# Kernel tuning notes

Hardware: AMD Instinct MI355X
Metric: run time of the kernel (lower is better)

## Reference

```python
import jax, jax.numpy as jnp
import numpy as np

D_MODEL = 1024
N_HEADS = 16
D_K = D_MODEL // N_HEADS
SEQ = 2048
BATCH = 4


def setup_inputs() -> dict:
    key = jax.random.key(0)
    ks = jax.random.split(key, 11)
    s = 0.02
    inp = {
        'query': jax.random.normal(ks[0], (SEQ, BATCH, D_MODEL), jnp.float32),
        'key': jax.random.normal(ks[1], (SEQ, BATCH, D_MODEL), jnp.float32),
        'value': jax.random.normal(ks[2], (SEQ, BATCH, D_MODEL), jnp.float32),
        'Wq': jax.random.normal(ks[3], (D_MODEL, D_MODEL), jnp.float32) * s,
        'bq': jnp.zeros((D_MODEL,), jnp.float32),
        'Wk': jax.random.normal(ks[4], (D_MODEL, D_MODEL), jnp.float32) * s,
        'bk': jnp.zeros((D_MODEL,), jnp.float32),
        'Wv': jax.random.normal(ks[5], (D_MODEL, D_MODEL), jnp.float32) * s,
        'bv': jnp.zeros((D_MODEL,), jnp.float32),
        'Wo': jax.random.normal(ks[6], (D_MODEL, D_MODEL), jnp.float32) * s,
        'bo': jnp.zeros((D_MODEL,), jnp.float32),
    }
    return inp


def reference(query, key, value, Wq, bq, Wk, bk, Wv, bv, Wo, bo):
    # inputs are [S, B, D]; module transposes to batch-first
    q_in = jnp.swapaxes(query, 0, 1)  # [B, S, D]
    k_in = jnp.swapaxes(key, 0, 1)
    v_in = jnp.swapaxes(value, 0, 1)
    B, S, _ = q_in.shape
    # torch Linear: x @ W.T + b
    q = (q_in @ Wq.T + bq).reshape(B, S, N_HEADS, D_K)
    k = (k_in @ Wk.T + bk).reshape(B, S, N_HEADS, D_K)
    v = (v_in @ Wv.T + bv).reshape(B, S, N_HEADS, D_K)
    scale = jnp.sqrt(jnp.float32(D_K))
    scores = jnp.einsum('bqhd,bkhd->bhqk', q, k) / scale  # [B, H, S, S]
    attn = jax.nn.softmax(scores, axis=-1)
    # dropout is identity in eval / p=0
    context = jnp.einsum('bhqk,bkhd->bqhd', attn, v).reshape(B, S, D_MODEL)
    out = context @ Wo.T + bo  # [B, S, D]
    return jnp.swapaxes(out, 0, 1)  # back to [S, B, D]
```

## Files before the change

kernel.cpp:

```cpp
#include <hip/hip_runtime.h>
#include <math.h>

typedef unsigned short u16;
typedef unsigned int   u32;
typedef float f32x4  __attribute__((ext_vector_type(4)));
typedef float f32x16 __attribute__((ext_vector_type(16)));
typedef __bf16 bf16x8 __attribute__((ext_vector_type(8)));
typedef __bf16 bf16x2 __attribute__((ext_vector_type(2)));

#define SEQ   2048
#define BATCH 4
#define NH    16
#define DK    64
#define DM    1024
#define MTOT  (SEQ*BATCH)
#define SCL_QK 0.18033688011116016f

#if __has_builtin(__builtin_amdgcn_exp2f)
#define EXP2(x) __builtin_amdgcn_exp2f(x)
#else
#define EXP2(x) exp2f(x)
#endif

static __device__ __forceinline__ u16 f2bf(float f) {
  __bf16 h = (__bf16)f;
  return __builtin_bit_cast(u16, h);
}
static __device__ __forceinline__ u32 pk2(float a, float b) {
  bf16x2 t = {(__bf16)a, (__bf16)b};
  return __builtin_bit_cast(u32, t);
}

typedef __attribute__((address_space(1))) const void g1_t;
typedef __attribute__((address_space(3))) void l3_t;
static __device__ __forceinline__ void gload16(const void* g, void* l) {
  __builtin_amdgcn_global_load_lds((g1_t*)g, (l3_t*)l, 16, 0, 0);
}

static __device__ __forceinline__ void cast8(const float* __restrict__ src,
                                             u16* __restrict__ dst, int i) {
  float4 a = ((const float4*)src)[2 * i];
  float4 b = ((const float4*)src)[2 * i + 1];
  uint4 r;
  r.x = pk2(a.x, a.y); r.y = pk2(a.z, a.w);
  r.z = pk2(b.x, b.y); r.w = pk2(b.z, b.w);
  ((uint4*)dst)[i] = r;
}

__global__ __launch_bounds__(256)
void cast_bf16(const float* __restrict__ src, u16* __restrict__ dst, int n8) {
  int i = blockIdx.x * 256 + threadIdx.x;
  if (i < n8) cast8(src, dst, i);
}

__global__ __launch_bounds__(256)
void cast_w(const float* __restrict__ Wq, const float* __restrict__ Wk,
            const float* __restrict__ Wv, const float* __restrict__ Wo,
            u16* __restrict__ w3, u16* __restrict__ wo_c) {
  int bid = blockIdx.x;
  int t = bid >> 9, idx = bid & 511;
  const float* src = (t == 0) ? Wq : (t == 1) ? Wk : (t == 2) ? Wv : Wo;
  u16* dst = (t < 3) ? (w3 + (size_t)t * DM * DM) : wo_c;
  cast8(src, dst, idx * 256 + threadIdx.x);
}

__global__ __launch_bounds__(256)
void cast_all(const float* __restrict__ q, const float* __restrict__ k,
              const float* __restrict__ v,
              const float* __restrict__ Wq, const float* __restrict__ Wk,
              const float* __restrict__ Wv, const float* __restrict__ Wo,
              u16* __restrict__ in_c, u16* __restrict__ w3, u16* __restrict__ wo_c) {
  int bid = blockIdx.x;
  const float* src; u16* dst; int idx;
  if (bid < 12288) {
    int t = bid >> 12; idx = bid & 4095;
    src = (t == 0) ? q : (t == 1) ? k : v;
    dst = in_c + (size_t)t * MTOT * DM;
  } else {
    int wb = bid - 12288;
    int t = wb >> 9; idx = wb & 511;
    src = (t == 0) ? Wq : (t == 1) ? Wk : (t == 2) ? Wv : Wo;
    dst = (t < 3) ? (w3 + (size_t)t * DM * DM) : wo_c;
  }
  cast8(src, dst, idx * 256 + threadIdx.x);
}

template<int OGEMM>
__global__ __launch_bounds__(256, 4)
void gemm_k(const u16* __restrict__ a0, const u16* __restrict__ a1,
            const u16* __restrict__ a2, const u16* __restrict__ w3,
            const float* __restrict__ b0, const float* __restrict__ b1,
            const float* __restrict__ b2,
            u16* __restrict__ o0, u16* __restrict__ o1, u16* __restrict__ o2,
            float* __restrict__ o3, int seg_base)
{
  constexpr int BM = 128, BN = 128, BK = 32;
  __shared__ u16 As[BM * BK];
  __shared__ u16 Bs[BN * BK];

  const int seg = OGEMM ? 0 : (seg_base + (int)(blockIdx.x >> 3));
  const int n0  = OGEMM ? blockIdx.x * BN : (blockIdx.x & 7) * BN;
  const int m0  = blockIdx.y * BM;
  const u16* A = OGEMM ? a0 : (seg == 0 ? a0 : seg == 1 ? a1 : a2);
  const u16* W = OGEMM ? w3 : (w3 + (size_t)seg * DM * DM);
  const float* bias = OGEMM ? b0 : (seg == 0 ? b0 : seg == 1 ? b1 : b2);

  const int tid  = threadIdx.x;
  const int w    = tid >> 6;
  const int lane = tid & 63;
  const int quad = lane >> 4;
  const int l15  = lane & 15;
  const int wm = (w >> 1) * 64;
  const int wn = (w & 1) * 64;

  size_t aoff[2], woff[2];
  for (int p = 0; p < 2; p++) {
    int row = w * 32 + p * 16 + (lane >> 2);
    int gm = m0 + row;
    if (OGEMM) {
      aoff[p] = (size_t)gm * DM + (lane & 3) * 8;
    } else {
      int bb = gm >> 11, s = gm & (SEQ - 1);
      aoff[p] = (size_t)(s * BATCH + bb) * DM + (lane & 3) * 8;
    }
    woff[p] = (size_t)(n0 + row) * DM + (lane & 3) * 8;
  }

  f32x4 zero4 = {0.f, 0.f, 0.f, 0.f};
  f32x4 acc[4][4];
  for (int i = 0; i < 4; i++)
    for (int j = 0; j < 4; j++)
      acc[i][j] = zero4;

  for (int k0 = 0; k0 < DM; k0 += BK) {
    for (int p = 0; p < 2; p++) {
      gload16(A + aoff[p] + k0, &As[(w * 32 + p * 16) * BK]);
      gload16(W + woff[p] + k0, &Bs[(w * 32 + p * 16) * BK]);
    }
    __syncthreads();
    bf16x8 af[4], bfr[4];
    for (int i = 0; i < 4; i++)
      af[i] = *(const bf16x8*)&As[(wm + i * 16 + l15) * BK + quad * 8];
    for (int j = 0; j < 4; j++)
      bfr[j] = *(const bf16x8*)&Bs[(wn + j * 16 + l15) * BK + quad * 8];
    for (int i = 0; i < 4; i++)
      for (int j = 0; j < 4; j++)
        acc[i][j] = __builtin_amdgcn_mfma_f32_16x16x32_bf16(af[i], bfr[j], acc[i][j], 0, 0, 0);
    __syncthreads();
  }

  for (int j = 0; j < 4; j++) {
    int gn = n0 + wn + j * 16 + l15;
    float bv = bias[gn];
    int h = gn >> 6, dk = gn & 63;
    for (int i = 0; i < 4; i++) {
      int gmb = m0 + wm + i * 16 + quad * 4;
      for (int r = 0; r < 4; r++) {
        int gm = gmb + r;
        float val = acc[i][j][r] + bv;
        int bb = gm >> 11, s = gm & (SEQ - 1);
        if (OGEMM) {
          o3[(size_t)(s * BATCH + bb) * DM + gn] = val;
        } else if (seg == 0) {
          o0[((size_t)(bb * NH + h) * SEQ + s) * DK + dk] = f2bf(val * SCL_QK);
        } else if (seg == 1) {
          o1[((size_t)(bb * NH + h) * SEQ + s) * DK + dk] = f2bf(val);
        } else {
          o2[((size_t)(bb * NH + h) * DK + dk) * SEQ + s] = f2bf(val);
        }
      }
    }
  }
}

__global__ __launch_bounds__(256, 4)
void attn3(const u16* __restrict__ Q, const u16* __restrict__ K,
           const u16* __restrict__ VT, u16* __restrict__ ctx)
{
  __shared__ u16 Ks[2][64 * 64];
  __shared__ u16 Vs[2][64 * 64];

  const int bh = blockIdx.x;
  const int qt = blockIdx.y;
  const int b  = bh >> 4, h = bh & 15;
  const int tid  = threadIdx.x;
  const int w    = tid >> 6;
  const int lane = tid & 63;
  const int l31  = lane & 31;
  const int hi   = lane >> 5;

  const u16* Qb = Q  + (size_t)bh * SEQ * DK;
  const u16* Kb = K  + (size_t)bh * SEQ * DK;
  const u16* Vb = VT + (size_t)bh * DK * SEQ;

  const int qbase = qt * 128 + w * 32;
  const int qrow  = qbase + l31;

  bf16x8 qf[4];
#pragma unroll
  for (int ks = 0; ks < 4; ks++)
    qf[ks] = *(const bf16x8*)&Qb[(size_t)qrow * DK + ks * 16 + hi * 8];

  const int r0 = tid >> 3;
  const int sw = (tid & 7) ^ (r0 & 7);

#define STAGE(kbb, bufi) do {                                                       \
    _Pragma("unroll")                                                               \
    for (int p = 0; p < 2; p++) {                                                   \
      int row = p * 32 + r0;                                                        \
      gload16(&Kb[(size_t)((kbb) * 64 + row) * DK + sw * 8],                        \
              &Ks[bufi][(p * 32 + w * 8) * 64]);                                    \
      gload16(&Vb[(size_t)row * SEQ + (kbb) * 64 + sw * 8],                         \
              &Vs[bufi][(p * 32 + w * 8) * 64]);                                    \
    }                                                                               \
  } while (0)

  f32x16 z16;
#pragma unroll
  for (int i = 0; i < 16; i++) z16[i] = 0.f;

  f32x16 ot0 = z16, ot1 = z16;
  float2 ls2 = {0.f, 0.f};

  STAGE(0, 0);
  __syncthreads();

  for (int kb = 0; kb < SEQ / 64; kb++) {
    const int buf = kb & 1;
    if (kb + 1 < SEQ / 64) STAGE(kb + 1, buf ^ 1);

    const u16* KsB = &Ks[buf][0];
    const u16* VsB = &Vs[buf][0];

    f32x16 sa0 = z16, sa1 = z16;
#pragma unroll
    for (int ks = 0; ks < 4; ks++) {
      const int g0 = ((ks * 2 + hi) ^ (l31 & 7)) * 8;
      bf16x8 kf0 = *(const bf16x8*)&KsB[l31 * 64 + g0];
      bf16x8 kf1 = *(const bf16x8*)&KsB[(32 + l31) * 64 + g0];
      sa0 = __builtin_amdgcn_mfma_f32_32x32x16_bf16(kf0, qf[ks], sa0, 0, 0, 0);
      sa1 = __builtin_amdgcn_mfma_f32_32x32x16_bf16(kf1, qf[ks], sa1, 0, 0, 0);
    }

    u32 wp[8];

#define SOFTMAX_BLK(SA) do {                                                        \
    _Pragma("unroll")                                                               \
    for (int g = 0; g < 8; g++) {                                                   \
      float pa = EXP2(SA[2 * g]);                                                   \
      float pb = EXP2(SA[2 * g + 1]);                                               \
      ls2.x += pa; ls2.y += pb;                                                     \
      wp[g] = pk2(pa, pb);                                                          \
    }                                                                               \
  } while (0)

#define PVSTEP(KSB, KSL) do {                                                       \
    u32 a0 = wp[(KSB) * 4 + 0], a1 = wp[(KSB) * 4 + 1];                             \
    u32 a2 = wp[(KSB) * 4 + 2], a3 = wp[(KSB) * 4 + 3];                             \
    u32 s0 = hi ? a0 : a2, s1 = hi ? a1 : a3;                                       \
    u32 x0 = (u32)__shfl_xor((int)s0, 32);                                          \
    u32 x1 = (u32)__shfl_xor((int)s1, 32);                                          \
    uint4 pw;                                                                       \
    pw.x = hi ? x0 : a0; pw.y = hi ? x1 : a1;                                       \
    pw.z = hi ? a2 : x0; pw.w = hi ? a3 : x1;                                       \
    bf16x8 pf = __builtin_bit_cast(bf16x8, pw);                                     \
    const int gg = (((KSL) * 2 + hi) ^ (l31 & 7)) * 8;                              \
    bf16x8 vf0 = *(const bf16x8*)&VsB[l31 * 64 + gg];                               \
    bf16x8 vf1 = *(const bf16x8*)&VsB[(32 + l31) * 64 + gg];                        \
    ot0 = __builtin_amdgcn_mfma_f32_32x32x16_bf16(vf0, pf, ot0, 0, 0, 0);           \
    ot1 = __builtin_amdgcn_mfma_f32_32x32x16_bf16(vf1, pf, ot1, 0, 0, 0);           \
  } while (0)

    SOFTMAX_BLK(sa0);
    PVSTEP(0, 0);
    PVSTEP(1, 1);
    SOFTMAX_BLK(sa1);
    PVSTEP(0, 2);
    PVSTEP(1, 3);

    __syncthreads();
  }

  float ls = ls2.x + ls2.y;
  ls += __shfl_xor(ls, 32);
  float inv = 1.0f / ls;

  u16* crow = ctx + ((size_t)(b * SEQ + qrow)) * DM + h * DK;

#define STORE_BLK(OT, DKB) do {                                                     \
    _Pragma("unroll")                                                               \
    for (int t = 0; t < 4; t++) {                                                   \
      uint2 pr;                                                                     \
      pr.x = pk2(OT[4 * t + 0] * inv, OT[4 * t + 1] * inv);                         \
      pr.y = pk2(OT[4 * t + 2] * inv, OT[4 * t + 3] * inv);                         \
      *(uint2*)&crow[(DKB) * 32 + t * 8 + hi * 4] = pr;                             \
    }                                                                               \
  } while (0)

  STORE_BLK(ot0, 0);
  STORE_BLK(ot1, 1);

#undef STAGE
#undef SOFTMAX_BLK
#undef PVSTEP
#undef STORE_BLK
}

extern "C" void kernel_launch(void* const* d_in, const int* in_sizes, int n_in,
                              void* d_out, int out_size, void* d_ws, size_t ws_size,
                              hipStream_t stream)
{
  const float* q  = (const float*)d_in[0];
  const float* k  = (const float*)d_in[1];
  const float* v  = (const float*)d_in[2];
  const float* Wq = (const float*)d_in[3];
  const float* bq = (const float*)d_in[4];
  const float* Wk = (const float*)d_in[5];
  const float* bk = (const float*)d_in[6];
  const float* Wv = (const float*)d_in[7];
  const float* bv = (const float*)d_in[8];
  const float* Wo = (const float*)d_in[9];
  const float* bo = (const float*)d_in[10];

  const size_t SZ_IN  = (size_t)MTOT * DM;
  const size_t SZ_W   = (size_t)DM * DM;
  const size_t NEED_FUSED = (3 * SZ_IN + 3 * SZ_W + SZ_W + 3 * SZ_IN) * 2;

  dim3 cblk(256);
  dim3 ggq(24, 64);
  dim3 ggs(8, 64);

  if (ws_size >= NEED_FUSED) {
    u16* in_c  = (u16*)d_ws;
    u16* w3    = in_c + 3 * SZ_IN;
    u16* wo_c  = w3   + 3 * SZ_W;
    u16* q_ws  = wo_c + SZ_W;
    u16* k_ws  = q_ws + SZ_IN;
    u16* vt_ws = k_ws + SZ_IN;
    u16* ctx   = in_c;

    cast_all<<<14336, cblk, 0, stream>>>(q, k, v, Wq, Wk, Wv, Wo, in_c, w3, wo_c);
    gemm_k<0><<<ggq, cblk, 0, stream>>>(in_c, in_c + SZ_IN, in_c + 2 * SZ_IN, w3,
                                        bq, bk, bv, q_ws, k_ws, vt_ws, nullptr, 0);
    attn3<<<dim3(BATCH * NH, SEQ / 128), cblk, 0, stream>>>(q_ws, k_ws, vt_ws, ctx);
    gemm_k<1><<<ggs, cblk, 0, stream>>>(ctx, ctx, ctx, wo_c,
                                        bo, bo, bo, nullptr, nullptr, nullptr,
                                        (float*)d_out, 0);
  } else {
    u16* in_c  = (u16*)d_ws;
    u16* w3    = in_c + SZ_IN;
    u16* wo_c  = w3   + 3 * SZ_W;
    u16* q_ws  = wo_c + SZ_W;
    u16* k_ws  = q_ws + SZ_IN;
    u16* vt_ws = k_ws + SZ_IN;
    u16* ctx   = in_c;

    const int NA8 = MTOT * DM / 8;
    cast_w<<<2048, cblk, 0, stream>>>(Wq, Wk, Wv, Wo, w3, wo_c);
    cast_bf16<<<NA8 / 256, cblk, 0, stream>>>(q, in_c, NA8);
    gemm_k<0><<<ggs, cblk, 0, stream>>>(in_c, in_c, in_c, w3, bq, bk, bv,
                                        q_ws, k_ws, vt_ws, nullptr, 0);
    cast_bf16<<<NA8 / 256, cblk, 0, stream>>>(k, in_c, NA8);
    gemm_k<0><<<ggs, cblk, 0, stream>>>(in_c, in_c, in_c, w3, bq, bk, bv,
                                        q_ws, k_ws, vt_ws, nullptr, 1);
    cast_bf16<<<NA8 / 256, cblk, 0, stream>>>(v, in_c, NA8);
    gemm_k<0><<<ggs, cblk, 0, stream>>>(in_c, in_c, in_c, w3, bq, bk, bv,
                                        q_ws, k_ws, vt_ws, nullptr, 2);
    attn3<<<dim3(BATCH * NH, SEQ / 128), cblk, 0, stream>>>(q_ws, k_ws, vt_ws, ctx);
    gemm_k<1><<<ggs, cblk, 0, stream>>>(ctx, ctx, ctx, wo_c,
                                        bo, bo, bo, nullptr, nullptr, nullptr,
                                        (float*)d_out, 0);
  }
}
```

Measured before the change: 384.9 us.

## Double-buffer GEMM shared tiles and swizzle workgroup order

The projection GEMM now keeps two LDS buffers, so the global-to-LDS loads for the next K tile are issued before the MFMAs on the current tile. That removes one barrier per iteration and lets load latency overlap compute. It also remaps block IDs with a stride-8 swizzle, presumably to spread or group tiles for better L2 reuse across XCDs. The cost is doubled LDS per block, which could reduce occupancy under launch_bounds(256,4).

```diff
diff --git a/kernel.cpp b/kernel.cpp
--- a/kernel.cpp
+++ b/kernel.cpp
@@ -95,12 +95,18 @@
             float* __restrict__ o3, int seg_base)
 {
   constexpr int BM = 128, BN = 128, BK = 32;
-  __shared__ u16 As[BM * BK];
-  __shared__ u16 Bs[BN * BK];
-
-  const int seg = OGEMM ? 0 : (seg_base + (int)(blockIdx.x >> 3));
-  const int n0  = OGEMM ? blockIdx.x * BN : (blockIdx.x & 7) * BN;
-  const int m0  = blockIdx.y * BM;
+  __shared__ u16 As[2][BM * BK];
+  __shared__ u16 Bs[2][BN * BK];
+
+  const int nwg = gridDim.x * gridDim.y;
+  const int bid = blockIdx.y * gridDim.x + blockIdx.x;
+  const int swz = (bid & 7) * (nwg >> 3) + (bid >> 3);
+  const int bx  = swz % gridDim.x;
+  const int by  = swz / gridDim.x;
+
+  const int seg = OGEMM ? 0 : (seg_base + (bx >> 3));
+  const int n0  = OGEMM ? bx * BN : (bx & 7) * BN;
+  const int m0  = by * BM;
   const u16* A = OGEMM ? a0 : (seg == 0 ? a0 : seg == 1 ? a1 : a2);
   const u16* W = OGEMM ? w3 : (w3 + (size_t)seg * DM * DM);
   const float* bias = OGEMM ? b0 : (seg == 0 ? b0 : seg == 1 ? b1 : b2);
@@ -132,18 +138,34 @@
     for (int j = 0; j < 4; j++)
       acc[i][j] = zero4;
 
-  for (int k0 = 0; k0 < DM; k0 += BK) {
-    for (int p = 0; p < 2; p++) {
-      gload16(A + aoff[p] + k0, &As[(w * 32 + p * 16) * BK]);
-      gload16(W + woff[p] + k0, &Bs[(w * 32 + p * 16) * BK]);
+#pragma unroll
+  for (int p = 0; p < 2; p++) {
+    gload16(A + aoff[p], &As[0][(w * 32 + p * 16) * BK]);
+    gload16(W + woff[p], &Bs[0][(w * 32 + p * 16) * BK]);
+  }
+  __syncthreads();
+
+  constexpr int NKT = DM / BK;
+  for (int kt = 0; kt < NKT; kt++) {
+    const int cur = kt & 1;
+    if (kt + 1 < NKT) {
+      const int nk = (kt + 1) * BK;
+#pragma unroll
+      for (int p = 0; p < 2; p++) {
+        gload16(A + aoff[p] + nk, &As[cur ^ 1][(w * 32 + p * 16) * BK]);
+        gload16(W + woff[p] + nk, &Bs[cur ^ 1][(w * 32 + p * 16) * BK]);
+      }
     }
-    __syncthreads();
     bf16x8 af[4], bfr[4];
+#pragma unroll
     for (int i = 0; i < 4; i++)
-      af[i] = *(const bf16x8*)&As[(wm + i * 16 + l15) * BK + quad * 8];
+      af[i] = *(const bf16x8*)&As[cur][(wm + i * 16 + l15) * BK + quad * 8];
+#pragma unroll
     for (int j = 0; j < 4; j++)
-      bfr[j] = *(const bf16x8*)&Bs[(wn + j * 16 + l15) * BK + quad * 8];
+      bfr[j] = *(const bf16x8*)&Bs[cur][(wn + j * 16 + l15) * BK + quad * 8];
+#pragma unroll
     for (int i = 0; i < 4; i++)
+#pragma unroll
       for (int j = 0; j < 4; j++)
         acc[i][j] = __builtin_amdgcn_mfma_f32_16x16x32_bf16(af[i], bfr[j], acc[i][j], 0, 0, 0);
     __syncthreads();
```

Result: faster. 360.7 us (-6.3%).
